# Kernel tuning notes

Measured on AMD Instinct MI355X. Metric: run time of the kernel, lower is better.

## Reference

```python
import jax, jax.numpy as jnp
import numpy as np

EPS = 1e-5  # BatchNorm eps (torch default)

def setup_inputs() -> dict:
    key = jax.random.key(0)
    ks = jax.random.split(key, 24)
    B, NX, NY, F = 8, 128, 128, 128
    dims = [2 * F, 512, 256, 128, 64]
    d = {
        'x': jax.random.normal(ks[0], (B, NX, F), dtype=jnp.float32),
        'y': jax.random.normal(ks[1], (B, NY, F), dtype=jnp.float32),
    }
    i = 2
    for li, (din, dout) in enumerate(zip(dims[:-1], dims[1:]), start=1):
        d[f'w{li}'] = jax.random.normal(ks[i], (dout, din), dtype=jnp.float32) * (1.0 / np.sqrt(din)); i += 1
        d[f'b{li}'] = jax.random.normal(ks[i], (dout,), dtype=jnp.float32) * 0.02; i += 1
        if li < 4:  # BatchNorm1d on hidden layers only (eval mode: running stats)
            d[f'g{li}'] = 1.0 + 0.1 * jax.random.normal(ks[i], (dout,), dtype=jnp.float32); i += 1
            d[f'be{li}'] = 0.1 * jax.random.normal(ks[i], (dout,), dtype=jnp.float32); i += 1
            d[f'm{li}'] = 0.1 * jax.random.normal(ks[i], (dout,), dtype=jnp.float32); i += 1
            d[f'v{li}'] = 0.5 + jax.random.uniform(ks[i], (dout,), dtype=jnp.float32); i += 1
    return d

def _bn(h, g, be, m, v):
    # BatchNorm1d in eval mode over the channel (last) axis
    return (h - m) * (g * jax.lax.rsqrt(v + EPS)) + be

def reference(x, y,
              w1, b1, g1, be1, m1, v1,
              w2, b2, g2, be2, m2, v2,
              w3, b3, g3, be3, m3, v3,
              w4, b4):
    F = x.shape[-1]
    # First Linear on cat([x_i, y_j]) == split-weight broadcast add: avoids the
    # (B,nx,ny,2F) pairwise concat the torch code materializes (same math).
    wx, wy = w1[:, :F], w1[:, F:]                      # (512,F) each
    hx = jnp.einsum('bif,hf->bih', x, wx)              # (B,nx,512)
    hy = jnp.einsum('bjf,hf->bjh', y, wy)              # (B,ny,512)
    h = hx[:, :, None, :] + hy[:, None, :, :] + b1     # (B,nx,ny,512)
    h = jax.nn.relu(_bn(h, g1, be1, m1, v1))           # dropout is identity in eval
    h = jax.nn.relu(_bn(jnp.einsum('bijh,oh->bijo', h, w2) + b2, g2, be2, m2, v2))
    h = jax.nn.relu(_bn(jnp.einsum('bijh,oh->bijo', h, w3) + b3, g3, be3, m3, v3))
    e = jnp.einsum('bijh,oh->bijo', h, w4) + b4        # (B,nx,ny,64) embeddings
    # PSD path: einsum('bijk,bilk->bijl', e, e).sum(-1)
    #         == sum_k e[b,i,j,k] * (sum_l e[b,i,l,k])  -- avoids (B,nx,ny,ny)
    s = e.sum(axis=2)                                  # (B,nx,64)
    kernel = jnp.einsum('bijk,bik->bij', e, s)         # (B,nx,ny)
    return kernel
```

## Files before the change

kernel.cpp:

```cpp
#include <hip/hip_runtime.h>

#define EPS 1e-5f

typedef _Float16 half8 __attribute__((ext_vector_type(8)));
typedef _Float16 half4 __attribute__((ext_vector_type(4)));
typedef float f32x16 __attribute__((ext_vector_type(16)));
typedef float f32x4v __attribute__((ext_vector_type(4)));


__global__ __launch_bounds__(256)
void pre_kernel(
    const float* __restrict__ x, const float* __restrict__ y,
    const float* __restrict__ w1, const float* __restrict__ b1,
    const float* __restrict__ g1, const float* __restrict__ be1,
    const float* __restrict__ m1, const float* __restrict__ v1,
    const float* __restrict__ w2, const float* __restrict__ b2,
    const float* __restrict__ g2, const float* __restrict__ be2,
    const float* __restrict__ m2, const float* __restrict__ v2,
    const float* __restrict__ w3, const float* __restrict__ b3,
    const float* __restrict__ g3, const float* __restrict__ be3,
    const float* __restrict__ m3, const float* __restrict__ v3,
    const float* __restrict__ w4,
    _Float16* __restrict__ hxh, _Float16* __restrict__ hyh,
    _Float16* __restrict__ w2h, _Float16* __restrict__ w3h,
    _Float16* __restrict__ w4h,
    float* __restrict__ b2f, float* __restrict__ b3f)
{
    const int t = threadIdx.x;

    if (blockIdx.x >= 256) {
        int tid = (blockIdx.x - 256) * 256 + t;
        const int nth = 64 * 256;
        for (int idx = tid; idx < 256 * 512; idx += nth) {
            int n = idx >> 9, k = idx & 511;
            float a = g2[n] * rsqrtf(v2[n] + EPS);
            int addr = ((n >> 5) * 32 + (k >> 4)) * 512 + ((k >> 3) & 1) * 256 + (n & 31) * 8 + (k & 7);
            w2h[addr] = (_Float16)(a * w2[idx]);
        }
        for (int idx = tid; idx < 128 * 256; idx += nth) {
            int n = idx >> 8, k = idx & 255;
            float a = g3[n] * rsqrtf(v3[n] + EPS);
            int addr = ((n >> 5) * 16 + (k >> 4)) * 512 + ((k >> 3) & 1) * 256 + (n & 31) * 8 + (k & 7);
            w3h[addr] = (_Float16)(a * w3[idx]);
        }
        for (int idx = tid; idx < 64 * 128; idx += nth) {
            int n = idx >> 7, k = idx & 127;
            int addr = ((n >> 5) * 8 + (k >> 4)) * 512 + ((k >> 3) & 1) * 256 + (n & 31) * 8 + (k & 7);
            w4h[addr] = (_Float16)w4[idx];
        }
        if (tid < 256) {
            float a = g2[tid] * rsqrtf(v2[tid] + EPS);
            b2f[tid] = a * b2[tid] + be2[tid] - m2[tid] * a;
        } else if (tid < 384) {
            int n = tid - 256;
            float a = g3[n] * rsqrtf(v3[n] + EPS);
            b3f[n] = a * b3[n] + be3[n] - m3[n] * a;
        }
        return;
    }

    const int rg = blockIdx.x & 31;
    const int ng = (blockIdx.x >> 5) & 3;
    const int which = blockIdx.x >> 7;

    constexpr int LDA = 136;
    __shared__ _Float16 sh[32 * 136 + 128 * 136] __attribute__((aligned(16)));
    _Float16* xa = sh;
    _Float16* wb = sh + 32 * 136;

    const int rowbase = rg * 32;
    const float* src = which ? y : x;

#pragma unroll
    for (int p = 0; p < 4; ++p) {
        int c = p * 256 + t;
        int r = c >> 5, fo = (c & 31) * 4;
        f32x4v v = *(const f32x4v*)(src + (size_t)(rowbase + r) * 128 + fo);
        half4 h; h[0] = (_Float16)v[0]; h[1] = (_Float16)v[1];
        h[2] = (_Float16)v[2]; h[3] = (_Float16)v[3];
        *(half4*)(xa + r * LDA + fo) = h;
    }
#pragma unroll
    for (int p = 0; p < 16; ++p) {
        int c = p * 256 + t;
        int n = c >> 5, fo = (c & 31) * 4;
        f32x4v v = *(const f32x4v*)(w1 + (size_t)(ng * 128 + n) * 256 + which * 128 + fo);
        half4 h; h[0] = (_Float16)v[0]; h[1] = (_Float16)v[1];
        h[2] = (_Float16)v[2]; h[3] = (_Float16)v[3];
        *(half4*)(wb + n * LDA + fo) = h;
    }
    __syncthreads();

    const int wid = t >> 6;
    const int l = t & 63;
    const int l31 = l & 31, lh = l >> 5;

    f32x16 acc = (f32x16)0.f;
#pragma unroll
    for (int kc = 0; kc < 8; ++kc) {
        half8 af = *(const half8*)(xa + l31 * LDA + kc * 16 + lh * 8);
        half8 bf = *(const half8*)(wb + (wid * 32 + l31) * LDA + kc * 16 + lh * 8);
        acc = __builtin_amdgcn_mfma_f32_32x32x16_f16(af, bf, acc, 0, 0, 0);
    }

    const int n = ng * 128 + wid * 32 + l31;
    float alpha = g1[n] * rsqrtf(v1[n] + EPS);
    if (which == 0) {
        float bias = alpha * b1[n] + be1[n] - m1[n] * alpha;
#pragma unroll
        for (int r = 0; r < 16; ++r) {
            int m = (r & 3) + 8 * (r >> 2) + 4 * lh;
            hxh[(size_t)(rowbase + m) * 512 + n] = (_Float16)(alpha * acc[r] + bias);
        }
    } else {
        const int ks = n >> 4, lhh = (n >> 3) & 1, c = n & 7;
#pragma unroll
        for (int r = 0; r < 16; ++r) {
            int m = (r & 3) + 8 * (r >> 2) + 4 * lh;
            int R = rowbase + m;
            int bb = R >> 7, j = R & 127;
            int addr = bb * 65536 + ((j >> 5) * 32 + ks) * 512 + lhh * 256 + (j & 31) * 8 + c;
            hyh[addr] = (_Float16)(alpha * acc[r]);
        }
    }
}

__global__ __launch_bounds__(512, 4)
void fused_kernel(
    const _Float16* __restrict__ hxh, const _Float16* __restrict__ hyh,
    const _Float16* __restrict__ w2h, const _Float16* __restrict__ w3h,
    const _Float16* __restrict__ w4h,
    const float* __restrict__ b2f, const float* __restrict__ b3f,
    const float* __restrict__ b4,
    float* __restrict__ out)
{
    constexpr int LD2 = 264;
    constexpr int LD3 = 136;
    constexpr int LDE = 68;

    __shared__ char smem[3584 + 67584] __attribute__((aligned(16)));
    _Float16* hxs = (_Float16*)smem;
    float* spart  = (float*)(smem + 1024);
    float* ss     = (float*)(smem + 3072);
    char* R1 = smem + 3584;
    _Float16* a2  = (_Float16*)R1;
    _Float16* a3  = (_Float16*)R1;
    float*    es  = (float*)R1;

    const int b = blockIdx.x >> 7;
    const int i = blockIdx.x & 127;
    const int t = threadIdx.x;
    const int wid = t >> 6;
    const int l   = t & 63;
    const int l31 = l & 31;
    const int lh  = l >> 5;

    if (t < 64)
        *(half8*)(hxs + t * 8) = *(const half8*)(hxh + (size_t)(b * 128 + i) * 512 + t * 8);
    __syncthreads();

    const int wm2 = wid >> 1;
    const int wn2 = wid & 1;

    const _Float16* pa = hyh + (size_t)b * 65536 + (size_t)(wm2 * 32) * 512 + l * 8;
    const _Float16* pb = w2h + (size_t)(wn2 * 4) * 32 * 512 + l * 8;

    f32x16 c0 = (f32x16)(b2f[wn2 * 128 +  0 + l31]);
    f32x16 c1 = (f32x16)(b2f[wn2 * 128 + 32 + l31]);
    f32x16 c2 = (f32x16)(b2f[wn2 * 128 + 64 + l31]);
    f32x16 c3 = (f32x16)(b2f[wn2 * 128 + 96 + l31]);

    half8 A0, B00, B01, B02, B03;
    half8 A1, B10, B11, B12, B13;

    auto LD0 = [&](int ks) {
        A0  = *(const half8*)(pa + (size_t)ks * 512);
        B00 = *(const half8*)(pb + (size_t)(0 * 32 + ks) * 512);
        B01 = *(const half8*)(pb + (size_t)(1 * 32 + ks) * 512);
        B02 = *(const half8*)(pb + (size_t)(2 * 32 + ks) * 512);
        B03 = *(const half8*)(pb + (size_t)(3 * 32 + ks) * 512);
    };
    auto LD1 = [&](int ks) {
        A1  = *(const half8*)(pa + (size_t)ks * 512);
        B10 = *(const half8*)(pb + (size_t)(0 * 32 + ks) * 512);
        B11 = *(const half8*)(pb + (size_t)(1 * 32 + ks) * 512);
        B12 = *(const half8*)(pb + (size_t)(2 * 32 + ks) * 512);
        B13 = *(const half8*)(pb + (size_t)(3 * 32 + ks) * 512);
    };
    auto STEP0 = [&](int ks) {
        half8 rx = *(const half8*)(hxs + ks * 16 + lh * 8);
        half8 s = A0 + rx;
        half8 af;
#pragma unroll
        for (int c = 0; c < 8; ++c)
            af[c] = s[c] > (_Float16)0.f ? s[c] : (_Float16)0.f;
        c0 = __builtin_amdgcn_mfma_f32_32x32x16_f16(af, B00, c0, 0, 0, 0);
        c1 = __builtin_amdgcn_mfma_f32_32x32x16_f16(af, B01, c1, 0, 0, 0);
        c2 = __builtin_amdgcn_mfma_f32_32x32x16_f16(af, B02, c2, 0, 0, 0);
        c3 = __builtin_amdgcn_mfma_f32_32x32x16_f16(af, B03, c3, 0, 0, 0);
    };
    auto STEP1 = [&](int ks) {
        half8 rx = *(const half8*)(hxs + ks * 16 + lh * 8);
        half8 s = A1 + rx;
        half8 af;
#pragma unroll
        for (int c = 0; c < 8; ++c)
            af[c] = s[c] > (_Float16)0.f ? s[c] : (_Float16)0.f;
        c0 = __builtin_amdgcn_mfma_f32_32x32x16_f16(af, B10, c0, 0, 0, 0);
        c1 = __builtin_amdgcn_mfma_f32_32x32x16_f16(af, B11, c1, 0, 0, 0);
        c2 = __builtin_amdgcn_mfma_f32_32x32x16_f16(af, B12, c2, 0, 0, 0);
        c3 = __builtin_amdgcn_mfma_f32_32x32x16_f16(af, B13, c3, 0, 0, 0);
    };

    LD0(0);
#pragma unroll 2
    for (int ks = 0; ks < 32; ks += 2) {
        if (ks + 1 < 32) LD1(ks + 1);
        STEP0(ks);
        if (ks + 2 < 32) LD0(ks + 2);
        if (ks + 1 < 32) STEP1(ks + 1);
    }

#pragma unroll
    for (int r = 0; r < 16; ++r) {
        int m = wm2 * 32 + (r & 3) + 8 * (r >> 2) + 4 * lh;
        a2[m * LD2 + wn2 * 128 +  0 + l31] = (_Float16)fmaxf(c0[r], 0.f);
        a2[m * LD2 + wn2 * 128 + 32 + l31] = (_Float16)fmaxf(c1[r], 0.f);
        a2[m * LD2 + wn2 * 128 + 64 + l31] = (_Float16)fmaxf(c2[r], 0.f);
        a2[m * LD2 + wn2 * 128 + 96 + l31] = (_Float16)fmaxf(c3[r], 0.f);
    }
    __syncthreads();

    const int wm = wid >> 2, wn = wid & 3;
    f32x16 acc3[2];
    {
        float b3v = b3f[wn * 32 + l31];
        acc3[0] = (f32x16)b3v;
        acc3[1] = (f32x16)b3v;
    }
#pragma unroll 8
    for (int kc = 0; kc < 16; ++kc) {
        half8 bfr = *(const half8*)(w3h + (wn * 16 + kc) * 512 + l * 8);
        half8 af0 = *(const half8*)(a2 + (wm * 64 + l31) * LD2 + kc * 16 + lh * 8);
        half8 af1 = *(const half8*)(a2 + (wm * 64 + 32 + l31) * LD2 + kc * 16 + lh * 8);
        acc3[0] = __builtin_amdgcn_mfma_f32_32x32x16_f16(af0, bfr, acc3[0], 0, 0, 0);
        acc3[1] = __builtin_amdgcn_mfma_f32_32x32x16_f16(af1, bfr, acc3[1], 0, 0, 0);
    }
    __syncthreads();
#pragma unroll
    for (int mt = 0; mt < 2; ++mt)
#pragma unroll
        for (int r = 0; r < 16; ++r) {
            int m = wm * 64 + mt * 32 + (r & 3) + 8 * (r >> 2) + 4 * lh;
            a3[m * LD3 + wn * 32 + l31] = (_Float16)fmaxf(acc3[mt][r], 0.f);
        }
    __syncthreads();

    const int wm4 = wid >> 1, wn4 = wid & 1;
    f32x16 acc4 = (f32x16)(b4[wn4 * 32 + l31]);
#pragma unroll
    for (int kc = 0; kc < 8; ++kc) {
        half8 afr = *(const half8*)(a3 + (wm4 * 32 + l31) * LD3 + kc * 16 + lh * 8);
        half8 bfr = *(const half8*)(w4h + (wn4 * 8 + kc) * 512 + l * 8);
        acc4 = __builtin_amdgcn_mfma_f32_32x32x16_f16(afr, bfr, acc4, 0, 0, 0);
    }
    __syncthreads();
#pragma unroll
    for (int r = 0; r < 16; ++r) {
        int m = wm4 * 32 + (r & 3) + 8 * (r >> 2) + 4 * lh;
        es[m * LDE + wn4 * 32 + l31] = acc4[r];
    }
    __syncthreads();

    {
        float sv = 0.f;
#pragma unroll
        for (int jj = 0; jj < 16; ++jj) sv += es[(wid + jj * 8) * LDE + l];
        spart[wid * 64 + l] = sv;
    }
    __syncthreads();
    if (t < 64) {
        float s2 = 0.f;
#pragma unroll
        for (int r = 0; r < 8; ++r) s2 += spart[r * 64 + t];
        ss[t] = s2;
    }
    __syncthreads();
    {
        const int j = t >> 2, q = t & 3;
        float p = 0.f;
#pragma unroll
        for (int c = 0; c < 16; ++c) {
            int k = q + 4 * c;
            p += es[j * LDE + k] * ss[k];
        }
        p += __shfl_xor(p, 1);
        p += __shfl_xor(p, 2);
        if (q == 0) out[(size_t)(b * 128 + i) * 128 + j] = p;
    }
}

extern "C" void kernel_launch(void* const* d_in, const int* in_sizes, int n_in,
                              void* d_out, int out_size, void* d_ws, size_t ws_size,
                              hipStream_t stream)
{
    (void)in_sizes; (void)n_in; (void)out_size; (void)ws_size;

    const float* x   = (const float*)d_in[0];
    const float* y   = (const float*)d_in[1];
    const float* w1  = (const float*)d_in[2];
    const float* b1  = (const float*)d_in[3];
    const float* g1  = (const float*)d_in[4];
    const float* be1 = (const float*)d_in[5];
    const float* m1  = (const float*)d_in[6];
    const float* v1  = (const float*)d_in[7];
    const float* w2  = (const float*)d_in[8];
    const float* b2  = (const float*)d_in[9];
    const float* g2  = (const float*)d_in[10];
    const float* be2 = (const float*)d_in[11];
    const float* m2  = (const float*)d_in[12];
    const float* v2  = (const float*)d_in[13];
    const float* w3  = (const float*)d_in[14];
    const float* b3  = (const float*)d_in[15];
    const float* g3  = (const float*)d_in[16];
    const float* be3 = (const float*)d_in[17];
    const float* m3  = (const float*)d_in[18];
    const float* v3  = (const float*)d_in[19];
    const float* w4  = (const float*)d_in[20];
    const float* b4  = (const float*)d_in[21];
    float* out = (float*)d_out;

    float* b2f = (float*)d_ws;
    float* b3f = b2f + 256;
    _Float16* w2h = (_Float16*)(b3f + 128);
    _Float16* w3h = w2h + 131072;
    _Float16* w4h = w3h + 32768;
    _Float16* hxh = w4h + 8192;
    _Float16* hyh = hxh + 524288;

    hipLaunchKernelGGL(pre_kernel, dim3(320), dim3(256), 0, stream,
                       x, y, w1, b1, g1, be1, m1, v1,
                       w2, b2, g2, be2, m2, v2,
                       w3, b3, g3, be3, m3, v3,
                       w4,
                       hxh, hyh, w2h, w3h, w4h, b2f, b3f);

    hipLaunchKernelGGL(fused_kernel, dim3(1024), dim3(512), 0, stream,
                       hxh, hyh, w2h, w3h, w4h, b2f, b3f, b4, out);
}
```

Measured before the change: 68.84 us.

## Process two query rows per block to reuse hy and w2 operand loads

Each block of the fused kernel now handles two i rows instead of one, so the layer-2 GEMM loads of hy and w2 fragments are shared across both rows. Warps use a 2x2 tile with eight accumulators, and the later layers run twice in sequence through a shared tail routine. The grid is halved and launch bounds are relaxed to 2 blocks per SIMD group, which raises register pressure and lowers occupancy and block count, while the layers after layer 2 stay serialized per row.

```diff
diff --git a/kernel.cpp b/kernel.cpp
--- a/kernel.cpp
+++ b/kernel.cpp
@@ -125,7 +125,7 @@
     }
 }
 
-__global__ __launch_bounds__(512, 4)
+__global__ __launch_bounds__(512, 2)
 void fused_kernel(
     const _Float16* __restrict__ hxh, const _Float16* __restrict__ hyh,
     const _Float16* __restrict__ w2h, const _Float16* __restrict__ w3h,
@@ -138,78 +138,101 @@
     constexpr int LD3 = 136;
     constexpr int LDE = 68;
 
-    __shared__ char smem[3584 + 67584] __attribute__((aligned(16)));
+    __shared__ char smem[4352 + 67584] __attribute__((aligned(16)));
     _Float16* hxs = (_Float16*)smem;
-    float* spart  = (float*)(smem + 1024);
-    float* ss     = (float*)(smem + 3072);
-    char* R1 = smem + 3584;
+    float* spart  = (float*)(smem + 2048);
+    float* ss     = (float*)(smem + 4096);
+    char* R1 = smem + 4352;
     _Float16* a2  = (_Float16*)R1;
     _Float16* a3  = (_Float16*)R1;
     float*    es  = (float*)R1;
 
-    const int b = blockIdx.x >> 7;
-    const int i = blockIdx.x & 127;
+    const int b  = blockIdx.x >> 6;
+    const int ip = blockIdx.x & 63;
+    const int i0 = ip * 2;
     const int t = threadIdx.x;
     const int wid = t >> 6;
     const int l   = t & 63;
     const int l31 = l & 31;
     const int lh  = l >> 5;
 
-    if (t < 64)
-        *(half8*)(hxs + t * 8) = *(const half8*)(hxh + (size_t)(b * 128 + i) * 512 + t * 8);
+    if (t < 128) {
+        int iv = t >> 6;
+        *(half8*)(hxs + iv * 512 + (t & 63) * 8) =
+            *(const half8*)(hxh + (size_t)(b * 128 + i0 + iv) * 512 + (t & 63) * 8);
+    }
     __syncthreads();
 
-    const int wm2 = wid >> 1;
-    const int wn2 = wid & 1;
-
-    const _Float16* pa = hyh + (size_t)b * 65536 + (size_t)(wm2 * 32) * 512 + l * 8;
-    const _Float16* pb = w2h + (size_t)(wn2 * 4) * 32 * 512 + l * 8;
-
-    f32x16 c0 = (f32x16)(b2f[wn2 * 128 +  0 + l31]);
-    f32x16 c1 = (f32x16)(b2f[wn2 * 128 + 32 + l31]);
-    f32x16 c2 = (f32x16)(b2f[wn2 * 128 + 64 + l31]);
-    f32x16 c3 = (f32x16)(b2f[wn2 * 128 + 96 + l31]);
-
-    half8 A0, B00, B01, B02, B03;
-    half8 A1, B10, B11, B12, B13;
+    const int wm = wid >> 2, wn = wid & 3;
+
+    const _Float16* pa0 = hyh + (size_t)b * 65536 + (size_t)(2 * wm) * 32 * 512 + l * 8;
+    const _Float16* pa1 = pa0 + 32 * 512;
+    const _Float16* pb0 = w2h + (size_t)(2 * wn) * 32 * 512 + l * 8;
+    const _Float16* pb1 = pb0 + 32 * 512;
+
+    const float bb0 = b2f[wn * 64 + l31];
+    const float bb1 = b2f[wn * 64 + 32 + l31];
+    f32x16 d00 = (f32x16)bb0, d01 = (f32x16)bb1;
+    f32x16 d10 = (f32x16)bb0, d11 = (f32x16)bb1;
+    f32x16 e00 = (f32x16)bb0, e01 = (f32x16)bb1;
+    f32x16 e10 = (f32x16)bb0, e11 = (f32x16)bb1;
+
+    half8 A00, A01, B00, B01;
+    half8 A10, A11, B10, B11;
 
     auto LD0 = [&](int ks) {
-        A0  = *(const half8*)(pa + (size_t)ks * 512);
-        B00 = *(const half8*)(pb + (size_t)(0 * 32 + ks) * 512);
-        B01 = *(const half8*)(pb + (size_t)(1 * 32 + ks) * 512);
-        B02 = *(const half8*)(pb + (size_t)(2 * 32 + ks) * 512);
-        B03 = *(const half8*)(pb + (size_t)(3 * 32 + ks) * 512);
+        A00 = *(const half8*)(pa0 + (size_t)ks * 512);
+        A01 = *(const half8*)(pa1 + (size_t)ks * 512);
+        B00 = *(const half8*)(pb0 + (size_t)ks * 512);
+        B01 = *(const half8*)(pb1 + (size_t)ks * 512);
     };
     auto LD1 = [&](int ks) {
-        A1  = *(const half8*)(pa + (size_t)ks * 512);
-        B10 = *(const half8*)(pb + (size_t)(0 * 32 + ks) * 512);
-        B11 = *(const half8*)(pb + (size_t)(1 * 32 + ks) * 512);
-        B12 = *(const half8*)(pb + (size_t)(2 * 32 + ks) * 512);
-        B13 = *(const half8*)(pb + (size_t)(3 * 32 + ks) * 512);
-    };
-    auto STEP0 = [&](int ks) {
-        half8 rx = *(const half8*)(hxs + ks * 16 + lh * 8);
-        half8 s = A0 + rx;
+        A10 = *(const half8*)(pa0 + (size_t)ks * 512);
+        A11 = *(const half8*)(pa1 + (size_t)ks * 512);
+        B10 = *(const half8*)(pb0 + (size_t)ks * 512);
+        B11 = *(const half8*)(pb1 + (size_t)ks * 512);
+    };
+    auto RELU = [&](half8 a, half8 rx) {
+        half8 s = a + rx;
         half8 af;
 #pragma unroll
         for (int c = 0; c < 8; ++c)
             af[c] = s[c] > (_Float16)0.f ? s[c] : (_Float16)0.f;
-        c0 = __builtin_amdgcn_mfma_f32_32x32x16_f16(af, B00, c0, 0, 0, 0);
-        c1 = __builtin_amdgcn_mfma_f32_32x32x16_f16(af, B01, c1, 0, 0, 0);
-        c2 = __builtin_amdgcn_mfma_f32_32x32x16_f16(af, B02, c2, 0, 0, 0);
-        c3 = __builtin_amdgcn_mfma_f32_32x32x16_f16(af, B03, c3, 0, 0, 0);
+        return af;
+    };
+    auto STEP0 = [&](int ks) {
+        half8 rx0 = *(const half8*)(hxs + ks * 16 + lh * 8);
+        half8 rx1 = *(const half8*)(hxs + 512 + ks * 16 + lh * 8);
+        half8 af;
+        af = RELU(A00, rx0);
+        d00 = __builtin_amdgcn_mfma_f32_32x32x16_f16(af, B00, d00, 0, 0, 0);
+        d01 = __builtin_amdgcn_mfma_f32_32x32x16_f16(af, B01, d01, 0, 0, 0);
+        af = RELU(A01, rx0);
+        d10 = __builtin_amdgcn_mfma_f32_32x32x16_f16(af, B00, d10, 0, 0, 0);
+        d11 = __builtin_amdgcn_mfma_f32_32x32x16_f16(af, B01, d11, 0, 0, 0);
+        af = RELU(A00, rx1);
+        e00 = __builtin_amdgcn_mfma_f32_32x32x16_f16(af, B00, e00, 0, 0, 0);
+        e01 = __builtin_amdgcn_mfma_f32_32x32x16_f16(af, B01, e01, 0, 0, 0);
+        af = RELU(A01, rx1);
+        e10 = __builtin_amdgcn_mfma_f32_32x32x16_f16(af, B00, e10, 0, 0, 0);
+        e11 = __builtin_amdgcn_mfma_f32_32x32x16_f16(af, B01, e11, 0, 0, 0);
     };
     auto STEP1 = [&](int ks) {
-        half8 rx = *(const half8*)(hxs + ks * 16 + lh * 8);
-        half8 s = A1 + rx;
+        half8 rx0 = *(const half8*)(hxs + ks * 16 + lh * 8);
+        half8 rx1 = *(const half8*)(hxs + 512 + ks * 16 + lh * 8);
         half8 af;
-#pragma unroll
-        for (int c = 0; c < 8; ++c)
-            af[c] = s[c] > (_Float16)0.f ? s[c] : (_Float16)0.f;
-        c0 = __builtin_amdgcn_mfma_f32_32x32x16_f16(af, B10, c0, 0, 0, 0);
-        c1 = __builtin_amdgcn_mfma_f32_32x32x16_f16(af, B11, c1, 0, 0, 0);
-        c2 = __builtin_amdgcn_mfma_f32_32x32x16_f16(af, B12, c2, 0, 0, 0);
-        c3 = __builtin_amdgcn_mfma_f32_32x32x16_f16(af, B13, c3, 0, 0, 0);
+        af = RELU(A10, rx0);
+        d00 = __builtin_amdgcn_mfma_f32_32x32x16_f16(af, B10, d00, 0, 0, 0);
+        d01 = __builtin_amdgcn_mfma_f32_32x32x16_f16(af, B11, d01, 0, 0, 0);
+        af = RELU(A11, rx0);
+        d10 = __builtin_amdgcn_mfma_f32_32x32x16_f16(af, B10, d10, 0, 0, 0);
+        d11 = __builtin_amdgcn_mfma_f32_32x32x16_f16(af, B11, d11, 0, 0, 0);
+        af = RELU(A10, rx1);
+        e00 = __builtin_amdgcn_mfma_f32_32x32x16_f16(af, B10, e00, 0, 0, 0);
+        e01 = __builtin_amdgcn_mfma_f32_32x32x16_f16(af, B11, e01, 0, 0, 0);
+        af = RELU(A11, rx1);
+        e10 = __builtin_amdgcn_mfma_f32_32x32x16_f16(af, B10, e10, 0, 0, 0);
+        e11 = __builtin_amdgcn_mfma_f32_32x32x16_f16(af, B11, e11, 0, 0, 0);
     };
 
     LD0(0);
@@ -221,83 +244,89 @@
         if (ks + 1 < 32) STEP1(ks + 1);
     }
 
-#pragma unroll
-    for (int r = 0; r < 16; ++r) {
-        int m = wm2 * 32 + (r & 3) + 8 * (r >> 2) + 4 * lh;
-        a2[m * LD2 + wn2 * 128 +  0 + l31] = (_Float16)fmaxf(c0[r], 0.f);
-        a2[m * LD2 + wn2 * 128 + 32 + l31] = (_Float16)fmaxf(c1[r], 0.f);
-        a2[m * LD2 + wn2 * 128 + 64 + l31] = (_Float16)fmaxf(c2[r], 0.f);
-        a2[m * LD2 + wn2 * 128 + 96 + l31] = (_Float16)fmaxf(c3[r], 0.f);
-    }
-    __syncthreads();
-
-    const int wm = wid >> 2, wn = wid & 3;
-    f32x16 acc3[2];
-    {
-        float b3v = b3f[wn * 32 + l31];
-        acc3[0] = (f32x16)b3v;
-        acc3[1] = (f32x16)b3v;
-    }
-#pragma unroll 8
-    for (int kc = 0; kc < 16; ++kc) {
-        half8 bfr = *(const half8*)(w3h + (wn * 16 + kc) * 512 + l * 8);
-        half8 af0 = *(const half8*)(a2 + (wm * 64 + l31) * LD2 + kc * 16 + lh * 8);
-        half8 af1 = *(const half8*)(a2 + (wm * 64 + 32 + l31) * LD2 + kc * 16 + lh * 8);
-        acc3[0] = __builtin_amdgcn_mfma_f32_32x32x16_f16(af0, bfr, acc3[0], 0, 0, 0);
-        acc3[1] = __builtin_amdgcn_mfma_f32_32x32x16_f16(af1, bfr, acc3[1], 0, 0, 0);
-    }
-    __syncthreads();
-#pragma unroll
-    for (int mt = 0; mt < 2; ++mt)
+    auto TAIL = [&](const f32x16& a00, const f32x16& a01,
+                    const f32x16& a10, const f32x16& a11, int iv) {
 #pragma unroll
         for (int r = 0; r < 16; ++r) {
-            int m = wm * 64 + mt * 32 + (r & 3) + 8 * (r >> 2) + 4 * lh;
-            a3[m * LD3 + wn * 32 + l31] = (_Float16)fmaxf(acc3[mt][r], 0.f);
-        }
-    __syncthreads();
-
-    const int wm4 = wid >> 1, wn4 = wid & 1;
-    f32x16 acc4 = (f32x16)(b4[wn4 * 32 + l31]);
-#pragma unroll
-    for (int kc = 0; kc < 8; ++kc) {
-        half8 afr = *(const half8*)(a3 + (wm4 * 32 + l31) * LD3 + kc * 16 + lh * 8);
-        half8 bfr = *(const half8*)(w4h + (wn4 * 8 + kc) * 512 + l * 8);
-        acc4 = __builtin_amdgcn_mfma_f32_32x32x16_f16(afr, bfr, acc4, 0, 0, 0);
-    }
-    __syncthreads();
-#pragma unroll
-    for (int r = 0; r < 16; ++r) {
-        int m = wm4 * 32 + (r & 3) + 8 * (r >> 2) + 4 * lh;
-        es[m * LDE + wn4 * 32 + l31] = acc4[r];
-    }
-    __syncthreads();
-
-    {
-        float sv = 0.f;
-#pragma unroll
-        for (int jj = 0; jj < 16; ++jj) sv += es[(wid + jj * 8) * LDE + l];
-        spart[wid * 64 + l] = sv;
-    }
-    __syncthreads();
-    if (t < 64) {
-        float s2 = 0.f;
-#pragma unroll
-        for (int r = 0; r < 8; ++r) s2 += spart[r * 64 + t];
-        ss[t] = s2;
-    }
-    __syncthreads();
-    {
-        const int j = t >> 2, q = t & 3;
-        float p = 0.f;
-#pragma unroll
-        for (int c = 0; c < 16; ++c) {
-            int k = q + 4 * c;
-            p += es[j * LDE + k] * ss[k];
-        }
-        p += __shfl_xor(p, 1);
-        p += __shfl_xor(p, 2);
-        if (q == 0) out[(size_t)(b * 128 + i) * 128 + j] = p;
-    }
+            int m = wm * 64 + (r & 3) + 8 * (r >> 2) + 4 * lh;
+            a2[m * LD2 + wn * 64 + l31]               = (_Float16)fmaxf(a00[r], 0.f);
+            a2[m * LD2 + wn * 64 + 32 + l31]          = (_Float16)fmaxf(a01[r], 0.f);
+            a2[(m + 32) * LD2 + wn * 64 + l31]        = (_Float16)fmaxf(a10[r], 0.f);
+            a2[(m + 32) * LD2 + wn * 64 + 32 + l31]   = (_Float16)fmaxf(a11[r], 0.f);
+        }
+        __syncthreads();
+
+        f32x16 g0, g1;
+        {
+            float b3v = b3f[wn * 32 + l31];
+            g0 = (f32x16)b3v;
+            g1 = (f32x16)b3v;
+        }
+#pragma unroll 4
+        for (int kc = 0; kc < 16; ++kc) {
+            half8 bfr = *(const half8*)(w3h + (wn * 16 + kc) * 512 + l * 8);
+            half8 af0 = *(const half8*)(a2 + (wm * 64 + l31) * LD2 + kc * 16 + lh * 8);
+            half8 af1 = *(const half8*)(a2 + (wm * 64 + 32 + l31) * LD2 + kc * 16 + lh * 8);
+            g0 = __builtin_amdgcn_mfma_f32_32x32x16_f16(af0, bfr, g0, 0, 0, 0);
+            g1 = __builtin_amdgcn_mfma_f32_32x32x16_f16(af1, bfr, g1, 0, 0, 0);
+        }
+        __syncthreads();
+#pragma unroll
+        for (int mt = 0; mt < 2; ++mt)
+#pragma unroll
+            for (int r = 0; r < 16; ++r) {
+                int m = wm * 64 + mt * 32 + (r & 3) + 8 * (r >> 2) + 4 * lh;
+                a3[m * LD3 + wn * 32 + l31] = (_Float16)fmaxf(mt ? g1[r] : g0[r], 0.f);
+            }
+        __syncthreads();
+
+        const int wm4 = wid >> 1, wn4 = wid & 1;
+        f32x16 acc4 = (f32x16)(b4[wn4 * 32 + l31]);
+#pragma unroll
+        for (int kc = 0; kc < 8; ++kc) {
+            half8 afr = *(const half8*)(a3 + (wm4 * 32 + l31) * LD3 + kc * 16 + lh * 8);
+            half8 bfr = *(const half8*)(w4h + (wn4 * 8 + kc) * 512 + l * 8);
+            acc4 = __builtin_amdgcn_mfma_f32_32x32x16_f16(afr, bfr, acc4, 0, 0, 0);
+        }
+        __syncthreads();
+#pragma unroll
+        for (int r = 0; r < 16; ++r) {
+            int m = wm4 * 32 + (r & 3) + 8 * (r >> 2) + 4 * lh;
+            es[m * LDE + wn4 * 32 + l31] = acc4[r];
+        }
+        __syncthreads();
+
+        {
+            float sv = 0.f;
+#pragma unroll
+            for (int jj = 0; jj < 16; ++jj) sv += es[(wid + jj * 8) * LDE + l];
+            spart[wid * 64 + l] = sv;
+        }
+        __syncthreads();
+        if (t < 64) {
+            float s2 = 0.f;
+#pragma unroll
+            for (int r = 0; r < 8; ++r) s2 += spart[r * 64 + t];
+            ss[t] = s2;
+        }
+        __syncthreads();
+        {
+            const int j = t >> 2, q = t & 3;
+            float p = 0.f;
+#pragma unroll
+            for (int c = 0; c < 16; ++c) {
+                int k = q + 4 * c;
+                p += es[j * LDE + k] * ss[k];
+            }
+            p += __shfl_xor(p, 1);
+            p += __shfl_xor(p, 2);
+            if (q == 0) out[(size_t)(b * 128 + iv) * 128 + j] = p;
+        }
+        __syncthreads();
+    };
+
+    TAIL(d00, d01, d10, d11, i0);
+    TAIL(e00, e01, e10, e11, i0 + 1);
 }
 
 extern "C" void kernel_launch(void* const* d_in, const int* in_sizes, int n_in,
@@ -345,6 +374,6 @@
                        w4,
                        hxh, hyh, w2h, w3h, w4h, b2f, b3f);
 
-    hipLaunchKernelGGL(fused_kernel, dim3(1024), dim3(512), 0, stream,
+    hipLaunchKernelGGL(fused_kernel, dim3(512), dim3(512), 0, stream,
                        hxh, hyh, w2h, w3h, w4h, b2f, b3f, b4, out);
 }
```

New measurement: 67.21 us. -2.4%, faster.
